# Performance work log

Hardware: AMD Instinct MI355X
Metric: run time of the kernel (lower is better)

The kernel has to match this reference:

```python
import jax, jax.numpy as jnp
import numpy as np

NEG_SLOPE = 0.2


def gatv2_layer(x, edge_index, Wl, Wr, att, bias):
    """PyG GATv2Conv (share_weights=False, concat=True, negative_slope=0.2).
    x: [N, F]; Wl/Wr: [F, H*C]; att: [H, C]; bias: [H*C]. Returns [N, H*C]."""
    N = x.shape[0]
    H, C = att.shape
    src, dst = edge_index[0], edge_index[1]
    xl = (x @ Wl).reshape(N, H, C)  # source transform
    xr = (x @ Wr).reshape(N, H, C)  # target transform
    # per-edge attention logits
    e = jax.nn.leaky_relu(xl[src] + xr[dst], NEG_SLOPE)          # [E, H, C]
    logits = jnp.einsum('ehc,hc->eh', e, att)                     # [E, H]
    # segment softmax over incoming edges of each destination node
    m = jax.ops.segment_max(logits, dst, num_segments=N)          # [N, H]
    m = jnp.where(jnp.isfinite(m), m, 0.0)                        # empty segments
    ex = jnp.exp(logits - m[dst])                                 # [E, H]
    denom = jax.ops.segment_sum(ex, dst, num_segments=N)          # [N, H]
    alpha = ex / (denom[dst] + 1e-16)                             # [E, H]
    msg = xl[src] * alpha[..., None]                              # [E, H, C]
    out = jax.ops.segment_sum(msg, dst, num_segments=N)           # [N, H, C]
    return out.reshape(N, H * C) + bias


def setup_inputs() -> dict:
    key = jax.random.key(0)
    ks = jax.random.split(key, 10)
    N, E, F, H, C, OUT = 50000, 800000, 256, 8, 32, 64
    s = 0.05
    return {
        'x': jax.random.normal(ks[0], (N, F), dtype=jnp.float32),
        'edge_index': jax.random.randint(ks[1], (2, E), 0, N, dtype=jnp.int64),
        'Wl1': jax.random.normal(ks[2], (F, H * C), dtype=jnp.float32) * s,
        'Wr1': jax.random.normal(ks[3], (F, H * C), dtype=jnp.float32) * s,
        'att1': jax.random.normal(ks[4], (H, C), dtype=jnp.float32) * s,
        'b1': jax.random.normal(ks[5], (H * C,), dtype=jnp.float32) * s,
        'Wl2': jax.random.normal(ks[6], (H * C, OUT), dtype=jnp.float32) * s,
        'Wr2': jax.random.normal(ks[7], (H * C, OUT), dtype=jnp.float32) * s,
        'att2': jax.random.normal(ks[8], (1, OUT), dtype=jnp.float32) * s,
        'b2': jax.random.normal(ks[9], (OUT,), dtype=jnp.float32) * s,
    }


def reference(x, edge_index, Wl1, Wr1, att1, b1, Wl2, Wr2, att2, b2):
    h = gatv2_layer(x, edge_index, Wl1, Wr1, att1, b1)
    h = jax.nn.relu(h)
    h = gatv2_layer(h, edge_index, Wl2, Wr2, att2, b2)
    return (h, jax.nn.log_softmax(h, axis=1))
```

## Files before the change

### kernel.cpp

```cpp
#include <hip/hip_runtime.h>
#include <hip/hip_bf16.h>
#include <math.h>

#define NEG_SLOPE 0.2f

typedef __attribute__((ext_vector_type(8))) short short8;
typedef __attribute__((ext_vector_type(4))) float floatx4;
typedef __attribute__((ext_vector_type(2))) float floatx2;

__device__ inline ushort f2b(float f) {
    __hip_bfloat16 b = __float2bfloat16(f);
    return *(ushort*)&b;
}
__device__ inline floatx2 bf2x2(unsigned int d) {
    union { unsigned int i; float f; } lo, hi;
    lo.i = d << 16;
    hi.i = d & 0xffff0000u;
    floatx2 r = {lo.f, hi.f};
    return r;
}

#define GLOAD_LDS16(gp, lp)                                                    \
    __builtin_amdgcn_global_load_lds(                                          \
        (const __attribute__((address_space(1))) unsigned int*)(gp),           \
        (__attribute__((address_space(3))) unsigned int*)(lp), 16, 0, 0)

template<int BM, int BN, int KTOT>
__global__ __launch_bounds__(256) void gemm_bf16(const ushort* __restrict__ A,
                                                 const ushort* __restrict__ Bt,
                                                 ushort* __restrict__ C,
                                                 int M, int N)
{
    constexpr int WTM = (BN == 64) ? 32 : 64;
    constexpr int WM  = BM / WTM;
    constexpr int IT  = WTM / 16;
    constexpr int JT  = 4;
    __shared__ ushort As[BM * 32];
    __shared__ ushort Bs[BN * 32];
    const int tid = threadIdx.x;
    const int w = tid >> 6, lane = tid & 63;
    const int mw = (w % WM) * WTM;
    const int nw = (w / WM) * 64;
    const int m0 = blockIdx.y * BM;
    const int n0 = blockIdx.x * BN;
    const int lm = lane & 15;
    const int kg = lane >> 4;

    const int srow = tid >> 2, skc = tid & 3;

    const ushort* aSrc[BM / 64];
#pragma unroll
    for (int it = 0; it < BM / 64; ++it) {
        int grow = m0 + it * 64 + srow;
        if (grow >= M) grow = M - 1;
        aSrc[it] = A + (size_t)grow * KTOT + skc * 8;
    }
    const ushort* bSrc[BN / 64];
#pragma unroll
    for (int it = 0; it < BN / 64; ++it)
        bSrc[it] = Bt + (size_t)(n0 + it * 64 + srow) * KTOT + skc * 8;

    floatx4 acc[IT][JT];
#pragma unroll
    for (int i = 0; i < IT; ++i)
#pragma unroll
        for (int j = 0; j < JT; ++j) acc[i][j] = (floatx4)0.f;

#pragma unroll
    for (int k0 = 0; k0 < KTOT; k0 += 32) {
#pragma unroll
        for (int it = 0; it < BM / 64; ++it)
            GLOAD_LDS16(aSrc[it] + k0, As + (it * 256 + w * 64) * 8);
#pragma unroll
        for (int it = 0; it < BN / 64; ++it)
            GLOAD_LDS16(bSrc[it] + k0, Bs + (it * 256 + w * 64) * 8);
        __syncthreads();
        short8 a[IT], b[JT];
#pragma unroll
        for (int i = 0; i < IT; ++i)
            a[i] = *(const short8*)&As[(mw + i * 16 + lm) * 32 + kg * 8];
#pragma unroll
        for (int j = 0; j < JT; ++j)
            b[j] = *(const short8*)&Bs[(nw + j * 16 + lm) * 32 + kg * 8];
#pragma unroll
        for (int i = 0; i < IT; ++i)
#pragma unroll
            for (int j = 0; j < JT; ++j)
                acc[i][j] = __builtin_amdgcn_mfma_f32_16x16x32_bf16(a[i], b[j], acc[i][j], 0, 0, 0);
        __syncthreads();
    }

#pragma unroll
    for (int i = 0; i < IT; ++i) {
        int rbase = m0 + mw + i * 16 + (lane >> 4) * 4;
#pragma unroll
        for (int j = 0; j < JT; ++j) {
            int col = n0 + nw + j * 16 + lm;
#pragma unroll
            for (int r = 0; r < 4; ++r) {
                int row = rbase + r;
                if (row < M) C[(size_t)row * N + col] = f2b(acc[i][j][r]);
            }
        }
    }
}

__global__ void k_prep(const float* __restrict__ x, ushort* __restrict__ xb, int XB,
                       const float* __restrict__ Wl1, const float* __restrict__ Wr1,
                       const float* __restrict__ Wl2, const float* __restrict__ Wr2,
                       ushort* __restrict__ wlr1t, ushort* __restrict__ wlr2t,
                       const int* __restrict__ dst, int E, int* __restrict__ counts)
{
    const int b = blockIdx.x;
    const int t = threadIdx.x;
    if (b < XB) {
        int i = b * 2048 + t * 8;
        float4 f0 = *(const float4*)&x[i];
        float4 f1 = *(const float4*)&x[i + 4];
        short8 o;
        o[0] = (short)f2b(f0.x); o[1] = (short)f2b(f0.y);
        o[2] = (short)f2b(f0.z); o[3] = (short)f2b(f0.w);
        o[4] = (short)f2b(f1.x); o[5] = (short)f2b(f1.y);
        o[6] = (short)f2b(f1.z); o[7] = (short)f2b(f1.w);
        *(short8*)&xb[i] = o;
    } else if (b < XB + 640) {
        int i = (b - XB) * 256 + t;
        if (i < 65536) {
            int k = i >> 8, n = i & 255;
            wlr1t[n * 256 + k] = f2b(Wl1[i]);
        } else if (i < 131072) {
            int j = i - 65536;
            int k = j >> 8, n = j & 255;
            wlr1t[65536 + n * 256 + k] = f2b(Wr1[j]);
        } else if (i < 147456) {
            int j = i - 131072;
            int k = j >> 6, n = j & 63;
            wlr2t[n * 256 + k] = f2b(Wl2[j]);
        } else {
            int j = i - 147456;
            int k = j >> 6, n = j & 63;
            wlr2t[16384 + n * 256 + k] = f2b(Wr2[j]);
        }
    } else {
        int i = (b - XB - 640) * 256 + t;
        if (i < E) atomicAdd(&counts[dst[i]], 1);
    }
}

__global__ void k_chunksum(const int* __restrict__ counts, int N, int* __restrict__ chunk)
{
    __shared__ int sm[256];
    const int t = threadIdx.x;
    const int base = blockIdx.x * 1024;
    int s = 0;
    for (int i = t; i < 1024; i += 256) {
        int idx = base + i;
        s += (idx < N) ? counts[idx] : 0;
    }
    sm[t] = s;
    __syncthreads();
    for (int off = 128; off; off >>= 1) {
        if (t < off) sm[t] += sm[t + off];
        __syncthreads();
    }
    if (t == 0) chunk[blockIdx.x] = sm[0];
}

__global__ void k_scanfinish(const int* __restrict__ counts, int N,
                             const int* __restrict__ chunk, int nchunks,
                             int* __restrict__ offsets, int* __restrict__ cursor)
{
    __shared__ int sm[256];
    __shared__ int s_pref, s_total;
    const int t = threadIdx.x;
    if (t < 64) {
        int v = (t < nchunks) ? chunk[t] : 0;
        int inc = v;
#pragma unroll
        for (int off = 1; off < 64; off <<= 1) {
            int y = __shfl_up(inc, off);
            if (t >= off) inc += y;
        }
        if (t == (int)blockIdx.x) s_pref = inc - v;
        if (t == 63) s_total = inc;
    }
    __syncthreads();
    const int base = blockIdx.x * 1024 + t * 4;
    int v[4];
    int s = 0;
#pragma unroll
    for (int i = 0; i < 4; ++i) {
        v[i] = (base + i < N) ? counts[base + i] : 0;
        s += v[i];
    }
    sm[t] = s;
    __syncthreads();
    for (int off = 1; off < 256; off <<= 1) {
        int y = (t >= off) ? sm[t - off] : 0;
        __syncthreads();
        sm[t] += y;
        __syncthreads();
    }
    int run = s_pref + sm[t] - s;
#pragma unroll
    for (int i = 0; i < 4; ++i) {
        if (base + i < N) {
            offsets[base + i] = run;
            cursor[base + i] = run;
        }
        run += v[i];
    }
    if (blockIdx.x == 0 && t == 0) offsets[N] = s_total;
}

__global__ void k_fill(const int* __restrict__ src, const int* __restrict__ dst,
                       int E, int* __restrict__ cursor, int* __restrict__ csr_off)
{
    int i = blockIdx.x * blockDim.x + threadIdx.x;
    if (i < E) {
        int d = dst[i];
        int pos = atomicAdd(&cursor[d], 1);
        csr_off[pos] = src[i] * 1024;
    }
    if (i < 16) csr_off[E + i] = 0;
}

__global__ __launch_bounds__(256) void agg1(const ushort* __restrict__ xlr,
                                            const float* __restrict__ att,
                                            const float* __restrict__ bias,
                                            const int* __restrict__ offsets,
                                            const int* __restrict__ csr_off,
                                            ushort* __restrict__ h1, int N)
{
    const int wave = blockIdx.x * 4 + (threadIdx.x >> 6);
    const int lane = threadIdx.x & 63;
    if (wave >= N) return;
    const int n = wave;
    const int g = lane >> 5;
    const int sl = lane & 31;
    const int elem = (sl >> 2) * 32 + (sl & 3) * 8;
    const char* __restrict__ xbase = (const char*)xlr;
    const int ebyte = elem * 2;

    floatx2 attv2[4], xrv2[4];
    {
        uint4 xr8 = *(const uint4*)(xbase + (size_t)n * 1024 + 512 + ebyte);
        unsigned int xw[4] = {xr8.x, xr8.y, xr8.z, xr8.w};
#pragma unroll
        for (int i = 0; i < 4; ++i) {
            attv2[i] = *(const floatx2*)&att[elem + 2 * i];
            xrv2[i] = bf2x2(xw[i]);
        }
    }
    float m = -1e30f, l = 0.f;
    floatx2 acc2[4] = {(floatx2)0.f, (floatx2)0.f, (floatx2)0.f, (floatx2)0.f};

    const int beg = offsets[n], end = offsets[n + 1];
    uint4 vA, vB;
    int oC;
    {
        int k0 = beg + g;
        vA = *(const uint4*)(xbase + (unsigned)csr_off[k0] + ebyte);
        vB = *(const uint4*)(xbase + (unsigned)csr_off[k0 + 2] + ebyte);
        oC = csr_off[k0 + 4];
    }
    for (int kk = beg + g; kk < end; kk += 2) {
        uint4 cur = vA;
        vA = vB;
        vB = *(const uint4*)(xbase + (unsigned)oC + ebyte);
        oC = csr_off[kk + 6];

        unsigned int cw[4] = {cur.x, cur.y, cur.z, cur.w};
        floatx2 xl2[4];
        floatx2 u2 = (floatx2)0.f;
#pragma unroll
        for (int i = 0; i < 4; ++i) {
            xl2[i] = bf2x2(cw[i]);
            floatx2 t = xl2[i] + xrv2[i];
            t = __builtin_elementwise_max(t, t * NEG_SLOPE);
            u2 += t * attv2[i];
        }
        float u = u2.x + u2.y;
        u += __shfl_xor(u, 1);
        u += __shfl_xor(u, 2);
        float e = __expf(-fabsf(u - m));
        bool kp = (m >= u);
        float sc = kp ? 1.f : e;
        float p  = kp ? e : 1.f;
        m = fmaxf(m, u);
#pragma unroll
        for (int i = 0; i < 4; ++i) acc2[i] = acc2[i] * sc + xl2[i] * p;
        l = fmaf(l, sc, p);
    }
    {
        float mo = __shfl_xor(m, 32);
        float lo = __shfl_xor(l, 32);
        float nm = fmaxf(m, mo);
        float ea = __expf(m - nm);
        float eb = __expf(mo - nm);
#pragma unroll
        for (int i = 0; i < 4; ++i) {
            floatx2 ao = {__shfl_xor(acc2[i].x, 32), __shfl_xor(acc2[i].y, 32)};
            acc2[i] = acc2[i] * ea + ao * eb;
        }
        l = l * ea + lo * eb;
    }
    if (g == 0) {
        float rl = 1.f / (l + 1e-16f);
        short8 o;
#pragma unroll
        for (int i = 0; i < 4; ++i) {
            float v0 = fmaf(acc2[i].x, rl, bias[elem + 2 * i]);
            float v1 = fmaf(acc2[i].y, rl, bias[elem + 2 * i + 1]);
            o[2 * i]     = (short)f2b(fmaxf(v0, 0.f));
            o[2 * i + 1] = (short)f2b(fmaxf(v1, 0.f));
        }
        *(short8*)&h1[(size_t)n * 256 + elem] = o;
    }
}

__global__ __launch_bounds__(256) void agg2(const ushort* __restrict__ xlr,
                                            const float* __restrict__ att,
                                            const float* __restrict__ bias,
                                            const int* __restrict__ offsets,
                                            const int* __restrict__ csr_off,
                                            float* __restrict__ out, int N)
{
    const int wave = blockIdx.x * 4 + (threadIdx.x >> 6);
    const int lane = threadIdx.x & 63;
    if (wave >= N) return;
    const int n = wave;
    const int g = lane >> 3;
    const int cl = lane & 7;
    const char* __restrict__ xbase = (const char*)xlr;
    const int cbyte = cl * 16;

    floatx2 attv2[4], xrv2[4];
    {
        uint4 xr8 = *(const uint4*)(xbase + (size_t)n * 256 + 128 + cbyte);
        unsigned int xw[4] = {xr8.x, xr8.y, xr8.z, xr8.w};
#pragma unroll
        for (int i = 0; i < 4; ++i) {
            attv2[i] = *(const floatx2*)&att[cl * 8 + 2 * i];
            xrv2[i] = bf2x2(xw[i]);
        }
    }
    float m = -1e30f, l = 0.f;
    floatx2 acc2[4] = {(floatx2)0.f, (floatx2)0.f, (floatx2)0.f, (floatx2)0.f};

    const int beg = offsets[n], end = offsets[n + 1];
    uint4 vA;
    int oB;
    {
        int k0 = beg + g;
        vA = *(const uint4*)(xbase + ((unsigned)csr_off[k0] >> 2) + cbyte);
        oB = csr_off[k0 + 8];
    }
    for (int kk = beg + g; kk < end; kk += 8) {
        uint4 cur = vA;
        vA = *(const uint4*)(xbase + ((unsigned)oB >> 2) + cbyte);
        oB = csr_off[kk + 16];

        unsigned int cw[4] = {cur.x, cur.y, cur.z, cur.w};
        floatx2 xl2[4];
        floatx2 u2 = (floatx2)0.f;
#pragma unroll
        for (int i = 0; i < 4; ++i) {
            xl2[i] = bf2x2(cw[i]);
            floatx2 t = xl2[i] + xrv2[i];
            t = __builtin_elementwise_max(t, t * NEG_SLOPE);
            u2 += t * attv2[i];
        }
        float u = u2.x + u2.y;
        u += __shfl_xor(u, 1);
        u += __shfl_xor(u, 2);
        u += __shfl_xor(u, 4);
        float e = __expf(-fabsf(u - m));
        bool kp = (m >= u);
        float sc = kp ? 1.f : e;
        float p  = kp ? e : 1.f;
        m = fmaxf(m, u);
#pragma unroll
        for (int i = 0; i < 4; ++i) acc2[i] = acc2[i] * sc + xl2[i] * p;
        l = fmaf(l, sc, p);
    }
#pragma unroll
    for (int off = 8; off <= 32; off <<= 1) {
        float mo = __shfl_xor(m, off);
        float lo = __shfl_xor(l, off);
        float nm = fmaxf(m, mo);
        float sa = __expf(m - nm);
        float sb = __expf(mo - nm);
#pragma unroll
        for (int i = 0; i < 4; ++i) {
            floatx2 ao = {__shfl_xor(acc2[i].x, off), __shfl_xor(acc2[i].y, off)};
            acc2[i] = acc2[i] * sa + ao * sb;
        }
        l = l * sa + lo * sb;
        m = nm;
    }
    float rl = 1.f / (l + 1e-16f);
    float h[8];
#pragma unroll
    for (int i = 0; i < 4; ++i) {
        h[2 * i]     = fmaf(acc2[i].x, rl, bias[cl * 8 + 2 * i]);
        h[2 * i + 1] = fmaf(acc2[i].y, rl, bias[cl * 8 + 2 * i + 1]);
    }

    float mx = h[0];
#pragma unroll
    for (int i = 1; i < 8; ++i) mx = fmaxf(mx, h[i]);
    mx = fmaxf(mx, __shfl_xor(mx, 1));
    mx = fmaxf(mx, __shfl_xor(mx, 2));
    mx = fmaxf(mx, __shfl_xor(mx, 4));
    float ssum = 0.f;
#pragma unroll
    for (int i = 0; i < 8; ++i) ssum += __expf(h[i] - mx);
    ssum += __shfl_xor(ssum, 1);
    ssum += __shfl_xor(ssum, 2);
    ssum += __shfl_xor(ssum, 4);
    float lg = mx + __logf(ssum);
    if (g == 0) {
        float4 o0 = make_float4(h[0], h[1], h[2], h[3]);
        float4 o1 = make_float4(h[4], h[5], h[6], h[7]);
        *(float4*)&out[(size_t)n * 64 + cl * 8] = o0;
        *(float4*)&out[(size_t)n * 64 + cl * 8 + 4] = o1;
        float4 s0 = make_float4(h[0] - lg, h[1] - lg, h[2] - lg, h[3] - lg);
        float4 s1 = make_float4(h[4] - lg, h[5] - lg, h[6] - lg, h[7] - lg);
        *(float4*)&out[(size_t)(N + n) * 64 + cl * 8] = s0;
        *(float4*)&out[(size_t)(N + n) * 64 + cl * 8 + 4] = s1;
    }
}

extern "C" void kernel_launch(void* const* d_in, const int* in_sizes, int n_in,
                              void* d_out, int out_size, void* d_ws, size_t ws_size,
                              hipStream_t stream)
{
    const float* x    = (const float*)d_in[0];
    const int*   ei   = (const int*)d_in[1];
    const float* Wl1  = (const float*)d_in[2];
    const float* Wr1  = (const float*)d_in[3];
    const float* att1 = (const float*)d_in[4];
    const float* b1   = (const float*)d_in[5];
    const float* Wl2  = (const float*)d_in[6];
    const float* Wr2  = (const float*)d_in[7];
    const float* att2 = (const float*)d_in[8];
    const float* b2   = (const float*)d_in[9];
    float* out = (float*)d_out;

    const int F = 256;
    const int E = in_sizes[1] / 2;
    const int N = in_sizes[0] / F;

    const int* e_src = ei;
    const int* e_dst = ei + E;

    ushort* xb    = (ushort*)d_ws;
    ushort* wlr1t = xb + (size_t)N * 256;
    ushort* wlr2t = wlr1t + 512 * 256;
    ushort* xlr1  = wlr2t + 128 * 256;
    ushort* h1b   = xlr1 + (size_t)N * 512;
    ushort* xlr2  = h1b + (size_t)N * 256;
    int* offsets  = (int*)(xlr2 + (size_t)N * 128);
    int* cursor   = offsets + (N + 1);
    int* counts   = cursor + (N + 1);
    int* chunkoff = counts + N;
    int* csr_off  = chunkoff + 66;

    const int nchunks = (N + 1023) / 1024;
    const int XB = (N * 256) / 2048;

    hipMemsetAsync(counts, 0, (size_t)N * sizeof(int), stream);
    k_prep<<<XB + 640 + (E + 255) / 256, 256, 0, stream>>>(
        x, xb, XB, Wl1, Wr1, Wl2, Wr2, wlr1t, wlr2t, e_dst, E, counts);

    gemm_bf16<128, 128, 256><<<dim3(4, (N + 127) / 128), 256, 0, stream>>>(xb, wlr1t, xlr1, N, 512);

    k_chunksum<<<nchunks, 256, 0, stream>>>(counts, N, chunkoff);
    k_scanfinish<<<nchunks, 256, 0, stream>>>(counts, N, chunkoff, nchunks, offsets, cursor);
    k_fill<<<(E + 255) / 256, 256, 0, stream>>>(e_src, e_dst, E, cursor, csr_off);

    agg1<<<(N + 3) / 4, 256, 0, stream>>>(xlr1, att1, b1, offsets, csr_off, h1b, N);

    gemm_bf16<128, 64, 256><<<dim3(2, (N + 127) / 128), 256, 0, stream>>>(h1b, wlr2t, xlr2, N, 128);
    agg2<<<(N + 3) / 4, 256, 0, stream>>>(xlr2, att2, b2, offsets, csr_off, out, N);
}
```

Before: 343.1 us.

## Pad GEMM LDS tiles, spread atomic counters, and pack two nodes per wave in agg2

The GEMM now loads tiles through registers into padded LDS rows (stride 40) instead of direct global-to-LDS loads, aiming to reduce bank conflicts on the MFMA operand reads. The per-node degree counters and cursors are spaced 16 ints apart to reduce atomic contention on shared cache lines, at the cost of a larger memset and strided scan reads. agg2 processes two destination nodes per wave with four edge groups each, to improve lane utilisation for low-degree nodes. The register-staged loads may cost extra VGPRs and instructions.

```diff
diff --git a/kernel.cpp b/kernel.cpp
--- a/kernel.cpp
+++ b/kernel.cpp
@@ -20,23 +20,19 @@
     return r;
 }
 
-#define GLOAD_LDS16(gp, lp)                                                    \
-    __builtin_amdgcn_global_load_lds(                                          \
-        (const __attribute__((address_space(1))) unsigned int*)(gp),           \
-        (__attribute__((address_space(3))) unsigned int*)(lp), 16, 0, 0)
-
 template<int BM, int BN, int KTOT>
 __global__ __launch_bounds__(256) void gemm_bf16(const ushort* __restrict__ A,
                                                  const ushort* __restrict__ Bt,
                                                  ushort* __restrict__ C,
                                                  int M, int N)
 {
+    constexpr int SA = 40;
     constexpr int WTM = (BN == 64) ? 32 : 64;
     constexpr int WM  = BM / WTM;
     constexpr int IT  = WTM / 16;
     constexpr int JT  = 4;
-    __shared__ ushort As[BM * 32];
-    __shared__ ushort Bs[BN * 32];
+    __shared__ ushort As[BM * SA];
+    __shared__ ushort Bs[BN * SA];
     const int tid = threadIdx.x;
     const int w = tid >> 6, lane = tid & 63;
     const int mw = (w % WM) * WTM;
@@ -69,19 +65,23 @@
 #pragma unroll
     for (int k0 = 0; k0 < KTOT; k0 += 32) {
 #pragma unroll
-        for (int it = 0; it < BM / 64; ++it)
-            GLOAD_LDS16(aSrc[it] + k0, As + (it * 256 + w * 64) * 8);
-#pragma unroll
-        for (int it = 0; it < BN / 64; ++it)
-            GLOAD_LDS16(bSrc[it] + k0, Bs + (it * 256 + w * 64) * 8);
+        for (int it = 0; it < BM / 64; ++it) {
+            short8 v = *(const short8*)(aSrc[it] + k0);
+            *(short8*)&As[(it * 64 + srow) * SA + skc * 8] = v;
+        }
+#pragma unroll
+        for (int it = 0; it < BN / 64; ++it) {
+            short8 v = *(const short8*)(bSrc[it] + k0);
+            *(short8*)&Bs[(it * 64 + srow) * SA + skc * 8] = v;
+        }
         __syncthreads();
         short8 a[IT], b[JT];
 #pragma unroll
         for (int i = 0; i < IT; ++i)
-            a[i] = *(const short8*)&As[(mw + i * 16 + lm) * 32 + kg * 8];
+            a[i] = *(const short8*)&As[(mw + i * 16 + lm) * SA + kg * 8];
 #pragma unroll
         for (int j = 0; j < JT; ++j)
-            b[j] = *(const short8*)&Bs[(nw + j * 16 + lm) * 32 + kg * 8];
+            b[j] = *(const short8*)&Bs[(nw + j * 16 + lm) * SA + kg * 8];
 #pragma unroll
         for (int i = 0; i < IT; ++i)
 #pragma unroll
@@ -109,7 +109,7 @@
                        const float* __restrict__ Wl1, const float* __restrict__ Wr1,
                        const float* __restrict__ Wl2, const float* __restrict__ Wr2,
                        ushort* __restrict__ wlr1t, ushort* __restrict__ wlr2t,
-                       const int* __restrict__ dst, int E, int* __restrict__ counts)
+                       const int* __restrict__ dst, int E, int* __restrict__ counts16)
 {
     const int b = blockIdx.x;
     const int t = threadIdx.x;
@@ -143,11 +143,11 @@
         }
     } else {
         int i = (b - XB - 640) * 256 + t;
-        if (i < E) atomicAdd(&counts[dst[i]], 1);
-    }
-}
-
-__global__ void k_chunksum(const int* __restrict__ counts, int N, int* __restrict__ chunk)
+        if (i < E) atomicAdd(&counts16[dst[i] * 16], 1);
+    }
+}
+
+__global__ void k_chunksum(const int* __restrict__ counts16, int N, int* __restrict__ chunk)
 {
     __shared__ int sm[256];
     const int t = threadIdx.x;
@@ -155,7 +155,7 @@
     int s = 0;
     for (int i = t; i < 1024; i += 256) {
         int idx = base + i;
-        s += (idx < N) ? counts[idx] : 0;
+        s += (idx < N) ? counts16[idx * 16] : 0;
     }
     sm[t] = s;
     __syncthreads();
@@ -166,9 +166,9 @@
     if (t == 0) chunk[blockIdx.x] = sm[0];
 }
 
-__global__ void k_scanfinish(const int* __restrict__ counts, int N,
+__global__ void k_scanfinish(const int* __restrict__ counts16, int N,
                              const int* __restrict__ chunk, int nchunks,
-                             int* __restrict__ offsets, int* __restrict__ cursor)
+                             int* __restrict__ offsets, int* __restrict__ cursor16)
 {
     __shared__ int sm[256];
     __shared__ int s_pref, s_total;
@@ -190,7 +190,7 @@
     int s = 0;
 #pragma unroll
     for (int i = 0; i < 4; ++i) {
-        v[i] = (base + i < N) ? counts[base + i] : 0;
+        v[i] = (base + i < N) ? counts16[(base + i) * 16] : 0;
         s += v[i];
     }
     sm[t] = s;
@@ -206,7 +206,7 @@
     for (int i = 0; i < 4; ++i) {
         if (base + i < N) {
             offsets[base + i] = run;
-            cursor[base + i] = run;
+            cursor16[(base + i) * 16] = run;
         }
         run += v[i];
     }
@@ -214,12 +214,12 @@
 }
 
 __global__ void k_fill(const int* __restrict__ src, const int* __restrict__ dst,
-                       int E, int* __restrict__ cursor, int* __restrict__ csr_off)
+                       int E, int* __restrict__ cursor16, int* __restrict__ csr_off)
 {
     int i = blockIdx.x * blockDim.x + threadIdx.x;
     if (i < E) {
         int d = dst[i];
-        int pos = atomicAdd(&cursor[d], 1);
+        int pos = atomicAdd(&cursor16[d * 16], 1);
         csr_off[pos] = src[i] * 1024;
     }
     if (i < 16) csr_off[E + i] = 0;
@@ -328,10 +328,11 @@
 {
     const int wave = blockIdx.x * 4 + (threadIdx.x >> 6);
     const int lane = threadIdx.x & 63;
-    if (wave >= N) return;
-    const int n = wave;
-    const int g = lane >> 3;
-    const int cl = lane & 7;
+    const int n = wave * 2 + (lane >> 5);
+    if (n >= N) return;
+    const int sub = lane & 31;
+    const int g = sub >> 3;
+    const int cl = sub & 7;
     const char* __restrict__ xbase = (const char*)xlr;
     const int cbyte = cl * 16;
 
@@ -354,12 +355,12 @@
     {
         int k0 = beg + g;
         vA = *(const uint4*)(xbase + ((unsigned)csr_off[k0] >> 2) + cbyte);
-        oB = csr_off[k0 + 8];
-    }
-    for (int kk = beg + g; kk < end; kk += 8) {
+        oB = csr_off[k0 + 4];
+    }
+    for (int kk = beg + g; kk < end; kk += 4) {
         uint4 cur = vA;
         vA = *(const uint4*)(xbase + ((unsigned)oB >> 2) + cbyte);
-        oB = csr_off[kk + 16];
+        oB = csr_off[kk + 8];
 
         unsigned int cw[4] = {cur.x, cur.y, cur.z, cur.w};
         floatx2 xl2[4];
@@ -385,7 +386,7 @@
         l = fmaf(l, sc, p);
     }
 #pragma unroll
-    for (int off = 8; off <= 32; off <<= 1) {
+    for (int off = 8; off <= 16; off <<= 1) {
         float mo = __shfl_xor(m, off);
         float lo = __shfl_xor(l, off);
         float nm = fmaxf(m, mo);
@@ -462,26 +463,26 @@
     ushort* h1b   = xlr1 + (size_t)N * 512;
     ushort* xlr2  = h1b + (size_t)N * 256;
     int* offsets  = (int*)(xlr2 + (size_t)N * 128);
-    int* cursor   = offsets + (N + 1);
-    int* counts   = cursor + (N + 1);
-    int* chunkoff = counts + N;
+    int* chunkoff = offsets + (N + 1);
     int* csr_off  = chunkoff + 66;
+    int* counts16 = csr_off + E + 16;
+    int* cursor16 = counts16 + (size_t)N * 16;
 
     const int nchunks = (N + 1023) / 1024;
     const int XB = (N * 256) / 2048;
 
-    hipMemsetAsync(counts, 0, (size_t)N * sizeof(int), stream);
+    hipMemsetAsync(counts16, 0, (size_t)N * 16 * sizeof(int), stream);
     k_prep<<<XB + 640 + (E + 255) / 256, 256, 0, stream>>>(
-        x, xb, XB, Wl1, Wr1, Wl2, Wr2, wlr1t, wlr2t, e_dst, E, counts);
+        x, xb, XB, Wl1, Wr1, Wl2, Wr2, wlr1t, wlr2t, e_dst, E, counts16);
 
     gemm_bf16<128, 128, 256><<<dim3(4, (N + 127) / 128), 256, 0, stream>>>(xb, wlr1t, xlr1, N, 512);
 
-    k_chunksum<<<nchunks, 256, 0, stream>>>(counts, N, chunkoff);
-    k_scanfinish<<<nchunks, 256, 0, stream>>>(counts, N, chunkoff, nchunks, offsets, cursor);
-    k_fill<<<(E + 255) / 256, 256, 0, stream>>>(e_src, e_dst, E, cursor, csr_off);
+    k_chunksum<<<nchunks, 256, 0, stream>>>(counts16, N, chunkoff);
+    k_scanfinish<<<nchunks, 256, 0, stream>>>(counts16, N, chunkoff, nchunks, offsets, cursor16);
+    k_fill<<<(E + 255) / 256, 256, 0, stream>>>(e_src, e_dst, E, cursor16, csr_off);
 
     agg1<<<(N + 3) / 4, 256, 0, stream>>>(xlr1, att1, b1, offsets, csr_off, h1b, N);
 
     gemm_bf16<128, 64, 256><<<dim3(2, (N + 127) / 128), 256, 0, stream>>>(h1b, wlr2t, xlr2, N, 128);
-    agg2<<<(N + 3) / 4, 256, 0, stream>>>(xlr2, att2, b2, offsets, csr_off, out, N);
-}
+    agg2<<<(N + 7) / 8, 256, 0, stream>>>(xlr2, att2, b2, offsets, csr_off, out, N);
+}
```

New measurement: 330.1 us. -3.8%, faster.
